# Performance work log

Hardware: AMD Instinct MI355X
Metric: run time of the kernel (lower is better)

The kernel has to match this reference:

```python
import jax, jax.numpy as jnp
import numpy as np
import math

SPARSITY = 0.95


def _linear(x, W, b):
    # torch nn.Linear: y = x @ W.T + b, W is [out, in]
    return jnp.einsum('bsd,od->bso', x, W) + b


def setup_inputs() -> dict:
    key = jax.random.key(0)
    ks = jax.random.split(key, 11)
    B, S, D = 2, 4096, 512
    std = 1.0 / math.sqrt(D)
    inp = {
        'x': jax.random.normal(ks[0], (B, S, D), dtype=jnp.float32),
        'mask_rand': jax.random.uniform(ks[1], (B, S, S), dtype=jnp.float32),
        'Wq': jax.random.normal(ks[2], (D, D), dtype=jnp.float32) * std,
        'bq': jax.random.normal(ks[3], (D,), dtype=jnp.float32) * std,
        'Wk': jax.random.normal(ks[4], (D, D), dtype=jnp.float32) * std,
        'bk': jax.random.normal(ks[5], (D,), dtype=jnp.float32) * std,
        'Wv': jax.random.normal(ks[6], (D, D), dtype=jnp.float32) * std,
        'bv': jax.random.normal(ks[7], (D,), dtype=jnp.float32) * std,
        'Wo': jax.random.normal(ks[8], (D, D), dtype=jnp.float32) * std,
        'bo': jax.random.normal(ks[9], (D,), dtype=jnp.float32) * std,
    }
    return inp


def reference(x, mask_rand, Wq, bq, Wk, bk, Wv, bv, Wo, bo):
    B, S, D = x.shape
    Q = _linear(x, Wq, bq)
    K = _linear(x, Wk, bk)
    V = _linear(x, Wv, bv)
    scores = jnp.einsum('bqd,bkd->bqk', Q, K) / jnp.sqrt(jnp.asarray(D, x.dtype))
    keep = mask_rand > SPARSITY  # random sparsity mask
    sparse_scores = jnp.where(keep, scores, -jnp.inf)
    attn = jax.nn.softmax(sparse_scores, axis=-1)
    attn_out = jnp.einsum('bqk,bkd->bqd', attn, V)
    # faithful to torch: transpose(1,2).contiguous().view(B, S, D)
    attn_out = jnp.swapaxes(attn_out, 1, 2).reshape(B, S, D)
    return _linear(attn_out, Wo, bo)
```

## Files before the change

kernel.cpp:

```cpp
#include <hip/hip_runtime.h>
#include <hip/hip_bf16.h>
#include <math.h>

typedef __bf16 bf16_t;
typedef __attribute__((ext_vector_type(8))) __bf16 bf16x8;
typedef __attribute__((ext_vector_type(4))) float f32x4;

constexpr int B_ = 2, S_ = 4096, D_ = 512;
constexpr int BS_ = B_ * S_;
constexpr int GRID_ = 512;
constexpr int NT_ = 256;
constexpr long QKV_E  = (long)BS_ * D_;
constexpr long W_E    = (long)D_ * D_;
constexpr long MASK_N = (long)BS_ * S_;
constexpr long CVT_UNITS  = (QKV_E + 4 * W_E) / 4;
constexpr long PACK_UNITS = MASK_N / 16;
constexpr float SCALE_ = 0.044194173824159216f;

__device__ __forceinline__ void load16_lds(const bf16_t* g, bf16_t* l) {
    __builtin_amdgcn_global_load_lds(
        (const __attribute__((address_space(1))) void*)g,
        (__attribute__((address_space(3))) void*)l, 16, 0, 0);
}

__device__ __forceinline__ void dev_cvt(long u,
    const float* x, const float* Wq, const float* Wk, const float* Wv,
    const float* Wo, bf16_t* dst)
{
    const long i = u * 4;
    const float* src; long o;
    if (i < QKV_E) { src = x; o = i; }
    else {
        const long j = i - QKV_E;
        const int w = (int)(j >> 18);
        o = j & (W_E - 1);
        src = (w == 0) ? Wq : (w == 1) ? Wk : (w == 2) ? Wv : Wo;
    }
    const float4 v = *(const float4*)(src + o);
    bf16_t out[4] = {(bf16_t)v.x, (bf16_t)v.y, (bf16_t)v.z, (bf16_t)v.w};
    *(uint2*)(dst + i) = *(uint2*)out;
}

__device__ __forceinline__ void dev_pack(long u,
    const float* mask, unsigned char* bm)
{
    const long i = u * 16;
    unsigned char o[16];
#pragma unroll
    for (int c = 0; c < 4; c++) {
        const float4 v = *(const float4*)(mask + i + c * 4);
        o[c * 4 + 0] = v.x > 0.95f;
        o[c * 4 + 1] = v.y > 0.95f;
        o[c * 4 + 2] = v.z > 0.95f;
        o[c * 4 + 3] = v.w > 0.95f;
    }
    *(uint4*)(bm + i) = *(uint4*)o;
}

__device__ __forceinline__ void kloop64(
    const bf16_t* At, const bf16_t* Bt, long ldA, long ldB, int kSteps,
    bf16_t* As, bf16_t* Bs, int tid, int wr, int wc, int quad, int r16,
    f32x4 (&acc)[4][4])
{
    const int srow = tid >> 3;
    const int cg = ((tid & 7) ^ (srow & 7)) * 8;
    const bf16_t* gA = At + (long)srow * ldA + cg;
    const bf16_t* gB = Bt + (long)srow * ldB + cg;
    bf16_t* lA = As + tid * 8;
    bf16_t* lB = Bs + tid * 8;

    for (int s = 0; s < kSteps; s++) {
        const int k0 = s * 64;
#pragma unroll
        for (int rr = 0; rr < 4; rr++) {
            load16_lds(gA + (long)rr * 32 * ldA + k0, lA + rr * 2048);
            load16_lds(gB + (long)rr * 32 * ldB + k0, lB + rr * 2048);
        }
        __syncthreads();
#pragma unroll
        for (int kh = 0; kh < 2; kh++) {
            bf16x8 af[4], bfr[4];
#pragma unroll
            for (int i = 0; i < 4; i++) {
                const int row = wr * 64 + i * 16 + r16;
                af[i] = *(const bf16x8*)(As + row * 64 +
                        (((kh << 2) + quad) ^ (row & 7)) * 8);
            }
#pragma unroll
            for (int j = 0; j < 4; j++) {
                const int row = wc * 64 + j * 16 + r16;
                bfr[j] = *(const bf16x8*)(Bs + row * 64 +
                        (((kh << 2) + quad) ^ (row & 7)) * 8);
            }
#pragma unroll
            for (int i = 0; i < 4; i++)
#pragma unroll
                for (int j = 0; j < 4; j++)
                    acc[i][j] = __builtin_amdgcn_mfma_f32_16x16x32_bf16(
                        af[i], bfr[j], acc[i][j], 0, 0, 0);
        }
        __syncthreads();
    }
}

__device__ __forceinline__ void dev_qkv_tile(int t,
    const bf16_t* Xc, const bf16_t* Wqc, const bf16_t* Wkc, const bf16_t* Wvc,
    const float* bq, const float* bk, const float* bv,
    bf16_t* Q, bf16_t* Kp, bf16_t* VT, char* smem, int tid)
{
    constexpr int K = 512;
    const int sel = t >> 8;
    const int tt  = t & 255;

    bf16_t* As = (bf16_t*)smem;
    bf16_t* Bs = As + 128 * 64;
    const int wave = tid >> 6, lane = tid & 63;
    const int quad = lane >> 4, r16 = lane & 15;
    const int wr = wave >> 1, wc = wave & 1;

    f32x4 acc[4][4] = {};

    if (sel < 2) {
        const int m0 = (tt >> 2) * 128;
        const int n0 = (tt & 3) * 128;
        const bf16_t* Bw = sel ? Wkc : Wqc;
        const float* bias = sel ? bk : bq;
        bf16_t* C = sel ? Kp : Q;
        kloop64(Xc + (long)m0 * K, Bw + (long)n0 * K, K, K, K / 64,
                As, Bs, tid, wr, wc, quad, r16, acc);
#pragma unroll
        for (int i = 0; i < 4; i++)
#pragma unroll
            for (int j = 0; j < 4; j++) {
                const int gn = n0 + wc * 64 + j * 16 + r16;
                const float bval = bias[gn];
#pragma unroll
                for (int reg = 0; reg < 4; reg++) {
                    const int gm = m0 + wr * 64 + i * 16 + quad * 4 + reg;
                    C[(long)gm * 512 + gn] = (bf16_t)(acc[i][j][reg] + bval);
                }
            }
    } else {
        const int m0 = (tt & 3) * 128;
        const int n0 = (tt >> 2) * 128;
        kloop64(Wvc + (long)m0 * K, Xc + (long)n0 * K, K, K, K / 64,
                As, Bs, tid, wr, wc, quad, r16, acc);
#pragma unroll
        for (int i = 0; i < 4; i++)
#pragma unroll
            for (int j = 0; j < 4; j++) {
                const int gn = n0 + wc * 64 + j * 16 + r16;
                const int b = gn >> 12, q = gn & 4095;
#pragma unroll
                for (int reg = 0; reg < 4; reg++) {
                    const int gm = m0 + wr * 64 + i * 16 + quad * 4 + reg;
                    VT[(long)b * D_ * S_ + (long)gm * S_ + q] =
                        (bf16_t)(acc[i][j][reg] + bv[gm]);
                }
            }
    }
}

__device__ __forceinline__ void dev_scores_tile(int t,
    const bf16_t* Q, const bf16_t* Kp, const unsigned char* bmask,
    bf16_t* SC, float* rowsum, char* smem, int tid)
{
    constexpr int S = S_, K = D_;
    const int x = t & 31;
    const int y = (t >> 5) & 31;
    const int b = t >> 10;
    const int m0 = y * 128, n0 = x * 128;

    bf16_t* As = (bf16_t*)smem;
    bf16_t* Bs = As + 128 * 64;
    const int wave = tid >> 6, lane = tid & 63;
    const int quad = lane >> 4, r16 = lane & 15;
    const int wr = wave >> 1, wc = wave & 1;

    f32x4 acc[4][4] = {};
    kloop64(Q + (long)b * S * K + (long)m0 * K,
            Kp + (long)b * S * K + (long)n0 * K, K, K, K / 64,
            As, Bs, tid, wr, wc, quad, r16, acc);

    float* wlds = (float*)smem + wave * 1088;
    const int erow = lane >> 2;
    const int ecg  = lane & 3;
    const long mbase = (long)b * S * S;

#pragma unroll
    for (int i = 0; i < 4; i++) {
#pragma unroll
        for (int j = 0; j < 4; j++)
#pragma unroll
            for (int reg = 0; reg < 4; reg++)
                wlds[(quad * 4 + reg) * 68 + j * 16 + r16] = acc[i][j][reg];
        __syncthreads();

        float v[16];
#pragma unroll
        for (int c = 0; c < 4; c++) {
            const float4 tv = *(const float4*)(wlds + erow * 68 + ecg * 16 + c * 4);
            v[c * 4 + 0] = tv.x; v[c * 4 + 1] = tv.y;
            v[c * 4 + 2] = tv.z; v[c * 4 + 3] = tv.w;
        }

        const int gm = m0 + wr * 64 + i * 16 + erow;
        const int gn = n0 + wc * 64 + ecg * 16;

        const uint4 mb = *(const uint4*)(bmask + mbase + (long)gm * S + gn);
        const unsigned char* mk = (const unsigned char*)&mb;
        float e[16];
#pragma unroll
        for (int tt = 0; tt < 16; tt++)
            e[tt] = mk[tt] ? __expf(v[tt] * SCALE_) : 0.f;

        bf16x8 o0, o1;
        float rsum = 0.f;
#pragma unroll
        for (int tt = 0; tt < 8; tt++) {
            rsum += e[tt] + e[tt + 8];
            o0[tt] = (bf16_t)e[tt];
            o1[tt] = (bf16_t)e[tt + 8];
        }
        bf16_t* cp = SC + mbase + (long)gm * S + gn;
        *(bf16x8*)cp       = o0;
        *(bf16x8*)(cp + 8) = o1;

        rsum += __shfl_xor(rsum, 1, 64);
        rsum += __shfl_xor(rsum, 2, 64);
        if (ecg == 0) atomicAdd(&rowsum[b * S + gm], rsum);
        __syncthreads();
    }
}

__device__ __forceinline__ void dev_pv_tile(int t,
    const bf16_t* VT, const bf16_t* SC, const float* rowsum,
    bf16_t* part, char* smem, int tid)
{
    constexpr int S = S_, D = D_;
    constexpr int KC = S / 2;
    const int x = t & 31;
    const int y = (t >> 5) & 3;
    const int z = t >> 7;
    const int b = z >> 1, ks = z & 1;
    const int m0 = y * 128, n0 = x * 128;
    const int kbeg = ks * KC;

    bf16_t* As = (bf16_t*)smem;
    bf16_t* Bs = As + 128 * 64;
    const int wave = tid >> 6, lane = tid & 63;
    const int quad = lane >> 4, r16 = lane & 15;
    const int wr = wave >> 1, wc = wave & 1;

    f32x4 acc[4][4] = {};
    kloop64(VT + (long)b * D * S + (long)m0 * S + kbeg,
            SC + (long)b * S * S + (long)n0 * S + kbeg, S, S, KC / 64,
            As, Bs, tid, wr, wc, quad, r16, acc);

    const long obase = ((long)ks * B_ + b) * (long)D * S;
#pragma unroll
    for (int i = 0; i < 4; i++)
#pragma unroll
        for (int j = 0; j < 4; j++) {
            const int gn = n0 + wc * 64 + j * 16 + r16;
            const float inv = 1.f / rowsum[b * S + gn];
#pragma unroll
            for (int reg = 0; reg < 4; reg++) {
                const int gm = m0 + wr * 64 + i * 16 + quad * 4 + reg;
                part[obase + (long)gm * S + gn] = (bf16_t)(acc[i][j][reg] * inv);
            }
        }
}

__device__ __forceinline__ void dev_out_tile(int t,
    const bf16_t* part, const bf16_t* Woc, const float* bo, float* C,
    char* smem, int tid)
{
    constexpr int N = 512, K = 512;
    const int m0 = (t >> 2) * 128, n0 = (t & 3) * 128;

    bf16_t* As = (bf16_t*)smem;
    bf16_t* Bs = As + 128 * 64;
    const int wave = tid >> 6, lane = tid & 63;
    const int quad = lane >> 4, r16 = lane & 15;
    const int wr = wave >> 1, wc = wave & 1;

    const int srow = tid >> 3;
    const int cg = ((tid & 7) ^ (srow & 7)) * 8;
    const bf16_t* gA0 = part + (long)(m0 + srow) * K + cg;
    const bf16_t* gA1 = gA0 + QKV_E;
    const bf16_t* gB  = Woc + (long)(n0 + srow) * K + cg;
    bf16_t* lA = As + tid * 8;
    bf16_t* lB = Bs + tid * 8;

    f32x4 acc[4][4] = {};

    for (int s = 0; s < K / 64; s++) {
        const int k0 = s * 64;
#pragma unroll
        for (int rr = 0; rr < 4; rr++) {
            const bf16x8 a0 = *(const bf16x8*)(gA0 + (long)rr * 32 * K + k0);
            const bf16x8 a1 = *(const bf16x8*)(gA1 + (long)rr * 32 * K + k0);
            bf16x8 sm;
#pragma unroll
            for (int e = 0; e < 8; e++)
                sm[e] = (bf16_t)((float)a0[e] + (float)a1[e]);
            *(bf16x8*)(lA + rr * 2048) = sm;
            load16_lds(gB + (long)rr * 32 * K + k0, lB + rr * 2048);
        }
        __syncthreads();
#pragma unroll
        for (int kh = 0; kh < 2; kh++) {
            bf16x8 af[4], bfr[4];
#pragma unroll
            for (int i = 0; i < 4; i++) {
                const int row = wr * 64 + i * 16 + r16;
                af[i] = *(const bf16x8*)(As + row * 64 +
                        (((kh << 2) + quad) ^ (row & 7)) * 8);
            }
#pragma unroll
            for (int j = 0; j < 4; j++) {
                const int row = wc * 64 + j * 16 + r16;
                bfr[j] = *(const bf16x8*)(Bs + row * 64 +
                        (((kh << 2) + quad) ^ (row & 7)) * 8);
            }
#pragma unroll
            for (int i = 0; i < 4; i++)
#pragma unroll
                for (int j = 0; j < 4; j++)
                    acc[i][j] = __builtin_amdgcn_mfma_f32_16x16x32_bf16(
                        af[i], bfr[j], acc[i][j], 0, 0, 0);
        }
        __syncthreads();
    }

#pragma unroll
    for (int i = 0; i < 4; i++)
#pragma unroll
        for (int j = 0; j < 4; j++) {
            const int gn = n0 + wc * 64 + j * 16 + r16;
            const float bval = bo[gn];
#pragma unroll
            for (int reg = 0; reg < 4; reg++) {
                const int gm = m0 + wr * 64 + i * 16 + quad * 4 + reg;
                C[(long)gm * N + gn] = acc[i][j][reg] + bval;
            }
        }
}

__global__ __launch_bounds__(256) void k_s1(
    const float* x, const float* mask, const float* Wq, const float* Wk,
    const float* Wv, const float* Wo, bf16_t* Xc, unsigned char* bmask,
    float* rowsum)
{
    const long gtid = (long)blockIdx.x * NT_ + threadIdx.x;
    for (long u = gtid; u < CVT_UNITS; u += (long)GRID_ * NT_)
        dev_cvt(u, x, Wq, Wk, Wv, Wo, Xc);
    for (long u = gtid; u < PACK_UNITS; u += (long)GRID_ * NT_)
        dev_pack(u, mask, bmask);
    if (gtid < BS_ / 4) {
        const float4 z = {0.f, 0.f, 0.f, 0.f};
        *(float4*)(rowsum + gtid * 4) = z;
    }
}

__global__ __launch_bounds__(256) void k_s2(
    const bf16_t* Xc, const float* bq, const float* bk, const float* bv,
    bf16_t* Q, bf16_t* Kp, bf16_t* VT)
{
    __shared__ char smem[32768];
    const bf16_t* Wqc = Xc + QKV_E;
    for (int t = blockIdx.x; t < 768; t += GRID_)
        dev_qkv_tile(t, Xc, Wqc, Wqc + W_E, Wqc + 2 * W_E,
                     bq, bk, bv, Q, Kp, VT, smem, threadIdx.x);
}

__global__ __launch_bounds__(256) void k_s3(
    const bf16_t* Q, const bf16_t* Kp, const unsigned char* bmask,
    bf16_t* SC, float* rowsum)
{
    __shared__ char smem[32768];
    for (int t = blockIdx.x; t < 2048; t += GRID_)
        dev_scores_tile(t, Q, Kp, bmask, SC, rowsum, smem, threadIdx.x);
}

__global__ __launch_bounds__(256) void k_s4(
    const bf16_t* VT, const bf16_t* SC, const float* rowsum, bf16_t* part)
{
    __shared__ char smem[32768];
    dev_pv_tile(blockIdx.x, VT, SC, rowsum, part, smem, threadIdx.x);
}

__global__ __launch_bounds__(256) void k_s6(
    const bf16_t* part, const bf16_t* Xc, const float* bo, float* C)
{
    __shared__ char smem[32768];
    const bf16_t* Woc = Xc + QKV_E + 3 * W_E;
    dev_out_tile(blockIdx.x, part, Woc, bo, C, smem, threadIdx.x);
}

extern "C" void kernel_launch(void* const* d_in, const int* in_sizes, int n_in,
                              void* d_out, int out_size, void* d_ws, size_t ws_size,
                              hipStream_t stream)
{
    const float* x    = (const float*)d_in[0];
    const float* mask = (const float*)d_in[1];
    const float* Wq   = (const float*)d_in[2];
    const float* bq   = (const float*)d_in[3];
    const float* Wk   = (const float*)d_in[4];
    const float* bk   = (const float*)d_in[5];
    const float* Wv   = (const float*)d_in[6];
    const float* bv   = (const float*)d_in[7];
    const float* Wo   = (const float*)d_in[8];
    const float* bo   = (const float*)d_in[9];
    float* outp = (float*)d_out;

    char* ws = (char*)d_ws;
    bf16_t* SC = (bf16_t*)ws;   ws += (long)BS_ * S_ * 2;
    bf16_t* VT = (bf16_t*)ws;   ws += QKV_E * 2;
    bf16_t* Q  = (bf16_t*)ws;   ws += QKV_E * 2;
    bf16_t* Kp = (bf16_t*)ws;   ws += QKV_E * 2;
    bf16_t* Xc = (bf16_t*)ws;   ws += (QKV_E + 4 * W_E) * 2;
    float* rowsum = (float*)ws; ws += (long)BS_ * 4;
    unsigned char* bmask = (unsigned char*)ws;
    bf16_t* part = (bf16_t*)ws;

    dim3 blk(NT_);
    k_s1<<<dim3(GRID_), blk, 0, stream>>>(x, mask, Wq, Wk, Wv, Wo,
                                          Xc, bmask, rowsum);
    k_s2<<<dim3(GRID_), blk, 0, stream>>>(Xc, bq, bk, bv, Q, Kp, VT);
    k_s3<<<dim3(GRID_), blk, 0, stream>>>(Q, Kp, bmask, SC, rowsum);
    k_s4<<<dim3(GRID_), blk, 0, stream>>>(VT, SC, rowsum, part);
    k_s6<<<dim3(256), blk, 0, stream>>>(part, Xc, bo, outp);
}
```

Baseline: 370.8 us.

## Read float mask directly in scores, split PV over four K chunks, swizzle blocks

```diff
diff --git a/kernel.cpp b/kernel.cpp
--- a/kernel.cpp
+++ b/kernel.cpp
@@ -8,19 +8,20 @@
 
 constexpr int B_ = 2, S_ = 4096, D_ = 512;
 constexpr int BS_ = B_ * S_;
-constexpr int GRID_ = 512;
 constexpr int NT_ = 256;
 constexpr long QKV_E  = (long)BS_ * D_;
 constexpr long W_E    = (long)D_ * D_;
-constexpr long MASK_N = (long)BS_ * S_;
-constexpr long CVT_UNITS  = (QKV_E + 4 * W_E) / 4;
-constexpr long PACK_UNITS = MASK_N / 16;
+constexpr long CVT_UNITS = (QKV_E + 4 * W_E) / 4;
 constexpr float SCALE_ = 0.044194173824159216f;
 
 __device__ __forceinline__ void load16_lds(const bf16_t* g, bf16_t* l) {
     __builtin_amdgcn_global_load_lds(
         (const __attribute__((address_space(1))) void*)g,
         (__attribute__((address_space(3))) void*)l, 16, 0, 0);
+}
+
+__device__ __forceinline__ int swz8(int bid, int chunk) {
+    return (bid & 7) * chunk + (bid >> 3);
 }
 
 __device__ __forceinline__ void dev_cvt(long u,
@@ -41,22 +42,6 @@
     *(uint2*)(dst + i) = *(uint2*)out;
 }
 
-__device__ __forceinline__ void dev_pack(long u,
-    const float* mask, unsigned char* bm)
-{
-    const long i = u * 16;
-    unsigned char o[16];
-#pragma unroll
-    for (int c = 0; c < 4; c++) {
-        const float4 v = *(const float4*)(mask + i + c * 4);
-        o[c * 4 + 0] = v.x > 0.95f;
-        o[c * 4 + 1] = v.y > 0.95f;
-        o[c * 4 + 2] = v.z > 0.95f;
-        o[c * 4 + 3] = v.w > 0.95f;
-    }
-    *(uint4*)(bm + i) = *(uint4*)o;
-}
-
 __device__ __forceinline__ void kloop64(
     const bf16_t* At, const bf16_t* Bt, long ldA, long ldB, int kSteps,
     bf16_t* As, bf16_t* Bs, int tid, int wr, int wc, int quad, int r16,
@@ -162,7 +147,7 @@
 }
 
 __device__ __forceinline__ void dev_scores_tile(int t,
-    const bf16_t* Q, const bf16_t* Kp, const unsigned char* bmask,
+    const bf16_t* Q, const bf16_t* Kp, const float* mask,
     bf16_t* SC, float* rowsum, char* smem, int tid)
 {
     constexpr int S = S_, K = D_;
@@ -207,12 +192,16 @@
         const int gm = m0 + wr * 64 + i * 16 + erow;
         const int gn = n0 + wc * 64 + ecg * 16;
 
-        const uint4 mb = *(const uint4*)(bmask + mbase + (long)gm * S + gn);
-        const unsigned char* mk = (const unsigned char*)&mb;
+        const float* mp = mask + mbase + (long)gm * S + gn;
         float e[16];
 #pragma unroll
-        for (int tt = 0; tt < 16; tt++)
-            e[tt] = mk[tt] ? __expf(v[tt] * SCALE_) : 0.f;
+        for (int c = 0; c < 4; c++) {
+            const float4 mk = *(const float4*)(mp + c * 4);
+            e[c * 4 + 0] = (mk.x > 0.95f) ? __expf(v[c * 4 + 0] * SCALE_) : 0.f;
+            e[c * 4 + 1] = (mk.y > 0.95f) ? __expf(v[c * 4 + 1] * SCALE_) : 0.f;
+            e[c * 4 + 2] = (mk.z > 0.95f) ? __expf(v[c * 4 + 2] * SCALE_) : 0.f;
+            e[c * 4 + 3] = (mk.w > 0.95f) ? __expf(v[c * 4 + 3] * SCALE_) : 0.f;
+        }
 
         bf16x8 o0, o1;
         float rsum = 0.f;
@@ -238,11 +227,11 @@
     bf16_t* part, char* smem, int tid)
 {
     constexpr int S = S_, D = D_;
-    constexpr int KC = S / 2;
+    constexpr int KC = S / 4;
     const int x = t & 31;
     const int y = (t >> 5) & 3;
     const int z = t >> 7;
-    const int b = z >> 1, ks = z & 1;
+    const int b = z >> 2, ks = z & 3;
     const int m0 = y * 128, n0 = x * 128;
     const int kbeg = ks * KC;
 
@@ -288,7 +277,6 @@
     const int srow = tid >> 3;
     const int cg = ((tid & 7) ^ (srow & 7)) * 8;
     const bf16_t* gA0 = part + (long)(m0 + srow) * K + cg;
-    const bf16_t* gA1 = gA0 + QKV_E;
     const bf16_t* gB  = Woc + (long)(n0 + srow) * K + cg;
     bf16_t* lA = As + tid * 8;
     bf16_t* lB = Bs + tid * 8;
@@ -300,11 +288,14 @@
 #pragma unroll
         for (int rr = 0; rr < 4; rr++) {
             const bf16x8 a0 = *(const bf16x8*)(gA0 + (long)rr * 32 * K + k0);
-            const bf16x8 a1 = *(const bf16x8*)(gA1 + (long)rr * 32 * K + k0);
+            const bf16x8 a1 = *(const bf16x8*)(gA0 + QKV_E + (long)rr * 32 * K + k0);
+            const bf16x8 a2 = *(const bf16x8*)(gA0 + 2 * QKV_E + (long)rr * 32 * K + k0);
+            const bf16x8 a3 = *(const bf16x8*)(gA0 + 3 * QKV_E + (long)rr * 32 * K + k0);
             bf16x8 sm;
 #pragma unroll
             for (int e = 0; e < 8; e++)
-                sm[e] = (bf16_t)((float)a0[e] + (float)a1[e]);
+                sm[e] = (bf16_t)((float)a0[e] + (float)a1[e] +
+                                 (float)a2[e] + (float)a3[e]);
             *(bf16x8*)(lA + rr * 2048) = sm;
             load16_lds(gB + (long)rr * 32 * K + k0, lB + rr * 2048);
         }
@@ -350,14 +341,11 @@
 
 __global__ __launch_bounds__(256) void k_s1(
     const float* x, const float* mask, const float* Wq, const float* Wk,
-    const float* Wv, const float* Wo, bf16_t* Xc, unsigned char* bmask,
-    float* rowsum)
+    const float* Wv, const float* Wo, bf16_t* Xc, float* rowsum)
 {
     const long gtid = (long)blockIdx.x * NT_ + threadIdx.x;
-    for (long u = gtid; u < CVT_UNITS; u += (long)GRID_ * NT_)
+    for (long u = gtid; u < CVT_UNITS; u += 1280L * NT_)
         dev_cvt(u, x, Wq, Wk, Wv, Wo, Xc);
-    for (long u = gtid; u < PACK_UNITS; u += (long)GRID_ * NT_)
-        dev_pack(u, mask, bmask);
     if (gtid < BS_ / 4) {
         const float4 z = {0.f, 0.f, 0.f, 0.f};
         *(float4*)(rowsum + gtid * 4) = z;
@@ -370,25 +358,24 @@
 {
     __shared__ char smem[32768];
     const bf16_t* Wqc = Xc + QKV_E;
-    for (int t = blockIdx.x; t < 768; t += GRID_)
-        dev_qkv_tile(t, Xc, Wqc, Wqc + W_E, Wqc + 2 * W_E,
-                     bq, bk, bv, Q, Kp, VT, smem, threadIdx.x);
+    dev_qkv_tile(swz8(blockIdx.x, 96), Xc, Wqc, Wqc + W_E, Wqc + 2 * W_E,
+                 bq, bk, bv, Q, Kp, VT, smem, threadIdx.x);
 }
 
 __global__ __launch_bounds__(256) void k_s3(
-    const bf16_t* Q, const bf16_t* Kp, const unsigned char* bmask,
+    const bf16_t* Q, const bf16_t* Kp, const float* mask,
     bf16_t* SC, float* rowsum)
 {
     __shared__ char smem[32768];
-    for (int t = blockIdx.x; t < 2048; t += GRID_)
-        dev_scores_tile(t, Q, Kp, bmask, SC, rowsum, smem, threadIdx.x);
+    dev_scores_tile(swz8(blockIdx.x, 256), Q, Kp, mask, SC, rowsum,
+                    smem, threadIdx.x);
 }
 
 __global__ __launch_bounds__(256) void k_s4(
     const bf16_t* VT, const bf16_t* SC, const float* rowsum, bf16_t* part)
 {
     __shared__ char smem[32768];
-    dev_pv_tile(blockIdx.x, VT, SC, rowsum, part, smem, threadIdx.x);
+    dev_pv_tile(swz8(blockIdx.x, 128), VT, SC, rowsum, part, smem, threadIdx.x);
 }
 
 __global__ __launch_bounds__(256) void k_s6(
@@ -396,7 +383,7 @@
 {
     __shared__ char smem[32768];
     const bf16_t* Woc = Xc + QKV_E + 3 * W_E;
-    dev_out_tile(blockIdx.x, part, Woc, bo, C, smem, threadIdx.x);
+    dev_out_tile(swz8(blockIdx.x, 32), part, Woc, bo, C, smem, threadIdx.x);
 }
 
 extern "C" void kernel_launch(void* const* d_in, const int* in_sizes, int n_in,
@@ -421,15 +408,13 @@
     bf16_t* Q  = (bf16_t*)ws;   ws += QKV_E * 2;
     bf16_t* Kp = (bf16_t*)ws;   ws += QKV_E * 2;
     bf16_t* Xc = (bf16_t*)ws;   ws += (QKV_E + 4 * W_E) * 2;
+    bf16_t* part = (bf16_t*)ws; ws += 4 * QKV_E * 2;
     float* rowsum = (float*)ws; ws += (long)BS_ * 4;
-    unsigned char* bmask = (unsigned char*)ws;
-    bf16_t* part = (bf16_t*)ws;
 
     dim3 blk(NT_);
-    k_s1<<<dim3(GRID_), blk, 0, stream>>>(x, mask, Wq, Wk, Wv, Wo,
-                                          Xc, bmask, rowsum);
-    k_s2<<<dim3(GRID_), blk, 0, stream>>>(Xc, bq, bk, bv, Q, Kp, VT);
-    k_s3<<<dim3(GRID_), blk, 0, stream>>>(Q, Kp, bmask, SC, rowsum);
-    k_s4<<<dim3(GRID_), blk, 0, stream>>>(VT, SC, rowsum, part);
-    k_s6<<<dim3(256), blk, 0, stream>>>(part, Xc, bo, outp);
-}
+    k_s1<<<dim3(1280), blk, 0, stream>>>(x, mask, Wq, Wk, Wv, Wo, Xc, rowsum);
+    k_s2<<<dim3(768),  blk, 0, stream>>>(Xc, bq, bk, bv, Q, Kp, VT);
+    k_s3<<<dim3(2048), blk, 0, stream>>>(Q, Kp, mask, SC, rowsum);
+    k_s4<<<dim3(1024), blk, 0, stream>>>(VT, SC, rowsum, part);
+    k_s6<<<dim3(256),  blk, 0, stream>>>(part, Xc, bo, outp);
+}
```

New measurement: 353.8 us. -4.6%, faster.
